# Kernel tuning notes

Hardware: AMD Instinct MI355X
Metric: run time of the kernel (lower is better)

The kernel has to match this reference:

```python
import jax, jax.numpy as jnp
import numpy as np

N_NODES = 100000
N_EDGES = 3200000
N_GRAPHS = 256
DIMS = [38, 64, 32, 16]


def setup_inputs() -> dict:
    key = jax.random.key(0)
    ks = jax.random.split(key, 16)
    x = jax.random.normal(ks[0], (N_NODES, DIMS[0]), dtype=jnp.float32)
    edge_index = jax.random.randint(ks[1], (2, N_EDGES), 0, N_NODES, dtype=jnp.int64)
    batch_vec = jnp.sort(jax.random.randint(ks[2], (N_NODES,), 0, N_GRAPHS, dtype=jnp.int64))
    inp = {"x": x, "edge_index": edge_index, "batch_vec": batch_vec}
    # Per layer l: W_rel [out,in] (with bias b [out]), W_root [out,in] (no bias)
    ki = 3
    for l in range(3):
        din, dout = DIMS[l], DIMS[l + 1]
        s = 1.0 / np.sqrt(din)
        inp[f"W_rel{l}"] = jax.random.uniform(ks[ki], (dout, din), minval=-s, maxval=s, dtype=jnp.float32); ki += 1
        inp[f"b{l}"] = jax.random.uniform(ks[ki], (dout,), minval=-s, maxval=s, dtype=jnp.float32); ki += 1
        inp[f"W_root{l}"] = jax.random.uniform(ks[ki], (dout, din), minval=-s, maxval=s, dtype=jnp.float32); ki += 1
    return inp


def _graph_conv(x, src, dst, W_rel, b, W_root):
    # sum_{j -> i} x_j, then linear (equivalent to summing transformed messages)
    agg = jax.ops.segment_sum(x[src], dst, num_segments=N_NODES)  # [N, din]
    return agg @ W_rel.T + b + x @ W_root.T


def reference(x, edge_index, batch_vec, W_rel0, b0, W_root0, W_rel1, b1, W_root1, W_rel2, b2, W_root2):
    src, dst = edge_index[0], edge_index[1]
    h = jnp.tanh(_graph_conv(x, src, dst, W_rel0, b0, W_root0))
    h = jnp.tanh(_graph_conv(h, src, dst, W_rel1, b1, W_root1))
    h = _graph_conv(h, src, dst, W_rel2, b2, W_root2)
    # global mean pool over graphs
    sums = jax.ops.segment_sum(h, batch_vec, num_segments=N_GRAPHS)  # [G, 16]
    counts = jax.ops.segment_sum(jnp.ones((N_NODES,), dtype=h.dtype), batch_vec, num_segments=N_GRAPHS)
    pooled = sums / jnp.maximum(counts, 1.0)[:, None]
    return jnp.tanh(pooled)
```

## Files before the change

### kernel.cpp

```cpp
#include <hip/hip_runtime.h>
#include <math.h>

#define N_NODES  100000
#define N_EDGES  3200000
#define N_GRAPHS 256


#define BSHIFT 9
#define NB 196
#define CAP 18432
#define NBLK 640
#define EPB ((N_EDGES + NBLK - 1) / NBLK)

typedef _Float16 f16;
typedef _Float16 f16x2 __attribute__((ext_vector_type(2)));

__device__ __forceinline__ float fast_tanh(float x) {
    x = fminf(20.f, fmaxf(-20.f, x));
    float e = __expf(2.f * x);
    return (e - 1.f) / (e + 1.f);
}

__device__ __forceinline__ unsigned int pack_bf2(float a, float b) {
    unsigned int ua = __float_as_uint(a);
    unsigned int ub = __float_as_uint(b);
    ua += 0x7fffu + ((ua >> 16) & 1u);
    ub += 0x7fffu + ((ub >> 16) & 1u);
    return (ua >> 16) | (ub & 0xffff0000u);
}

__device__ __forceinline__ f16x2 u2h(unsigned int u) { union { unsigned int u; f16x2 h; } c; c.u = u; return c.h; }
__device__ __forceinline__ unsigned int h2u(f16x2 h) { union { unsigned int u; f16x2 h; } c; c.h = h; return c.u; }
__device__ __forceinline__ unsigned int mkh2(float a, float b) {
    f16x2 v; v.x = (f16)a; v.y = (f16)b; return h2u(v);
}

__device__ __forceinline__ float fdot2f(f16x2 a, f16x2 b, float c) {
#if __has_builtin(__builtin_amdgcn_fdot2)
    return __builtin_amdgcn_fdot2(a, b, c, false);
#else
    return c + (float)a.x * (float)b.x + (float)a.y * (float)b.y;
#endif
}

__global__ __launch_bounds__(256) void k_scatter2(const int* __restrict__ src,
                                                  const int* __restrict__ dst,
                                                  int* __restrict__ bucket_cnt,
                                                  int* __restrict__ ebuf) {
    __shared__ int hist[NB];
    __shared__ int base[NB];
    __shared__ int cur[NB];
    int tid = threadIdx.x, b = blockIdx.x;
    for (int i = tid; i < NB; i += 256) { hist[i] = 0; cur[i] = 0; }
    __syncthreads();
    int lo = b * EPB, hi = min(lo + EPB, N_EDGES);
    for (int e = lo + tid; e < hi; e += 256)
        atomicAdd(&hist[((unsigned int)dst[e]) >> BSHIFT], 1);
    __syncthreads();
    for (int i = tid; i < NB; i += 256) {
        int c = hist[i];
        base[i] = (c > 0) ? atomicAdd(&bucket_cnt[i], c) : 0;
    }
    __syncthreads();
    for (int e = lo + tid; e < hi; e += 256) {
        int d = dst[e];
        int s = __builtin_nontemporal_load(src + e);
        int bin = d >> BSHIFT;
        int r = base[bin] + atomicAdd(&cur[bin], 1);
        if (r < CAP) ebuf[bin * CAP + r] = s | ((d & 511) << 17);
    }
}

__global__ __launch_bounds__(512) void k_bucket_csr2(const int* __restrict__ bucket_cnt,
                                                     int* __restrict__ ebuf,
                                                     int* __restrict__ rowptr,
                                                     int* __restrict__ rowend) {
    __shared__ int stage[CAP];
    __shared__ int cnt[512];
    __shared__ int cur[512];
    int b = blockIdx.x;
    int tid = threadIdx.x;
    int base = b * CAP;
    int n = min(bucket_cnt[b], CAP);
    cnt[tid] = 0;
    cur[tid] = 0;
    __syncthreads();
    for (int j = tid; j < n; j += 512) {
        int w = __builtin_nontemporal_load(ebuf + base + j);
        stage[j] = w;
        atomicAdd(&cnt[((unsigned int)w) >> 17], 1);
    }
    __syncthreads();
    int v = cnt[tid];
    int val = v;
    __syncthreads();
    cnt[tid] = val;
    __syncthreads();
#pragma unroll
    for (int o = 1; o < 512; o <<= 1) {
        int t = (tid >= o) ? cnt[tid - o] : 0;
        __syncthreads();
        val += t;
        cnt[tid] = val;
        __syncthreads();
    }
    int excl = val - v;
    int node = (b << BSHIFT) + tid;
    if (node < N_NODES) {
        rowptr[node] = base + excl;
        rowend[node] = base + val;
    }
    __syncthreads();
    for (int j = tid; j < n; j += 512) {
        int w = stage[j];
        int dl = ((unsigned int)w) >> 17;
        int off = (dl == 0) ? 0 : cnt[dl - 1];
        int r = atomicAdd(&cur[dl], 1);
        ebuf[base + off + r] = w & 0x1FFFF;
    }
}

__global__ __launch_bounds__(256) void k_cast_pad(const float* __restrict__ in,
                                                  unsigned int* __restrict__ out) {
    int i = blockIdx.x * 256 + threadIdx.x;
    if (i >= N_NODES * 20) return;
    int n = i / 20;
    int p = i - n * 20;
    unsigned int w = 0;
    if (p < 19) {
        float2 v = ((const float2*)in)[n * 19 + p];
        w = pack_bf2(v.x, v.y);
    }
    out[i] = w;
}

template<int NQ, int RSTRIDE, int ASTRIDE>
__global__ __launch_bounds__(256) void k_gather_quad(const unsigned int* __restrict__ feat,
                                                     const int* __restrict__ rowptr,
                                                     const int* __restrict__ rowend,
                                                     const int* __restrict__ elist,
                                                     float* __restrict__ agg) {
    int idx = blockIdx.x * 256 + threadIdx.x;
    if (idx >= N_NODES * NQ) return;
    int n = idx / NQ;
    int q = idx - n * NQ;
    int j = rowptr[n];
    int e = rowend[n];
    const unsigned int* fq = feat + q * 4;
    float a0 = 0.f, a1 = 0.f, a2 = 0.f, a3 = 0.f, a4 = 0.f, a5 = 0.f, a6 = 0.f, a7 = 0.f;
    for (; j + 3 < e; j += 4) {
        int s0 = __builtin_nontemporal_load(elist + j);
        int s1 = __builtin_nontemporal_load(elist + j + 1);
        int s2 = __builtin_nontemporal_load(elist + j + 2);
        int s3 = __builtin_nontemporal_load(elist + j + 3);
        uint4 w0 = *(const uint4*)(fq + (size_t)s0 * RSTRIDE);
        uint4 w1 = *(const uint4*)(fq + (size_t)s1 * RSTRIDE);
        uint4 w2 = *(const uint4*)(fq + (size_t)s2 * RSTRIDE);
        uint4 w3 = *(const uint4*)(fq + (size_t)s3 * RSTRIDE);
        a0 += __uint_as_float(w0.x << 16);
        a1 += __uint_as_float(w0.x & 0xffff0000u);
        a2 += __uint_as_float(w0.y << 16);
        a3 += __uint_as_float(w0.y & 0xffff0000u);
        a4 += __uint_as_float(w0.z << 16);
        a5 += __uint_as_float(w0.z & 0xffff0000u);
        a6 += __uint_as_float(w0.w << 16);
        a7 += __uint_as_float(w0.w & 0xffff0000u);
        a0 += __uint_as_float(w1.x << 16);
        a1 += __uint_as_float(w1.x & 0xffff0000u);
        a2 += __uint_as_float(w1.y << 16);
        a3 += __uint_as_float(w1.y & 0xffff0000u);
        a4 += __uint_as_float(w1.z << 16);
        a5 += __uint_as_float(w1.z & 0xffff0000u);
        a6 += __uint_as_float(w1.w << 16);
        a7 += __uint_as_float(w1.w & 0xffff0000u);
        a0 += __uint_as_float(w2.x << 16);
        a1 += __uint_as_float(w2.x & 0xffff0000u);
        a2 += __uint_as_float(w2.y << 16);
        a3 += __uint_as_float(w2.y & 0xffff0000u);
        a4 += __uint_as_float(w2.z << 16);
        a5 += __uint_as_float(w2.z & 0xffff0000u);
        a6 += __uint_as_float(w2.w << 16);
        a7 += __uint_as_float(w2.w & 0xffff0000u);
        a0 += __uint_as_float(w3.x << 16);
        a1 += __uint_as_float(w3.x & 0xffff0000u);
        a2 += __uint_as_float(w3.y << 16);
        a3 += __uint_as_float(w3.y & 0xffff0000u);
        a4 += __uint_as_float(w3.z << 16);
        a5 += __uint_as_float(w3.z & 0xffff0000u);
        a6 += __uint_as_float(w3.w << 16);
        a7 += __uint_as_float(w3.w & 0xffff0000u);
    }
    for (; j < e; ++j) {
        int s = __builtin_nontemporal_load(elist + j);
        uint4 w = *(const uint4*)(fq + (size_t)s * RSTRIDE);
        a0 += __uint_as_float(w.x << 16);
        a1 += __uint_as_float(w.x & 0xffff0000u);
        a2 += __uint_as_float(w.y << 16);
        a3 += __uint_as_float(w.y & 0xffff0000u);
        a4 += __uint_as_float(w.z << 16);
        a5 += __uint_as_float(w.z & 0xffff0000u);
        a6 += __uint_as_float(w.w << 16);
        a7 += __uint_as_float(w.w & 0xffff0000u);
    }
    float4* ao = (float4*)(agg + (size_t)n * ASTRIDE + q * 8);
    ao[0] = make_float4(a0, a1, a2, a3);
    ao[1] = make_float4(a4, a5, a6, a7);
}

__global__ __launch_bounds__(256) void k_fused0(const float* __restrict__ agg,
                                                const float* __restrict__ x,
                                                const float* __restrict__ Wrel0,
                                                const float* __restrict__ b0,
                                                const float* __restrict__ Wroot0,
                                                const float* __restrict__ Wrel1,
                                                const float* __restrict__ b1,
                                                const float* __restrict__ Wroot1,
                                                unsigned int* __restrict__ y1b,
                                                float* __restrict__ r1) {
    __shared__ unsigned int sWr[64 * 20];
    __shared__ unsigned int sWt[64 * 20];
    __shared__ unsigned int sW1r[32 * 32];
    __shared__ unsigned int sW1t[32 * 32];
    __shared__ float sb0[64];
    __shared__ float sb1[32];
    int tid = threadIdx.x;
    for (int i = tid; i < 64 * 20; i += 256) {
        int o = i / 20, d = i - o * 20;
        float a0 = (2 * d     < 38) ? Wrel0[o * 38 + 2 * d]     : 0.f;
        float a1 = (2 * d + 1 < 38) ? Wrel0[o * 38 + 2 * d + 1] : 0.f;
        float t0 = (2 * d     < 38) ? Wroot0[o * 38 + 2 * d]     : 0.f;
        float t1 = (2 * d + 1 < 38) ? Wroot0[o * 38 + 2 * d + 1] : 0.f;
        sWr[i] = mkh2(a0, a1);
        sWt[i] = mkh2(t0, t1);
    }
    for (int i = tid; i < 32 * 32; i += 256) {
        int op = i >> 5, j = i & 31;
        sW1r[i] = mkh2(Wrel1[j * 64 + 2 * op], Wrel1[j * 64 + 2 * op + 1]);
        sW1t[i] = mkh2(Wroot1[j * 64 + 2 * op], Wroot1[j * 64 + 2 * op + 1]);
    }
    if (tid < 64) sb0[tid] = b0[tid];
    if (tid < 32) sb1[tid] = b1[tid];
    __syncthreads();

    int lane = tid & 63;
    int ph = lane & 31;
    int sh = lane >> 5;
    int n0 = blockIdx.x * 256 + (tid >> 6) * 64 + 2 * ph;
    if (n0 >= N_NODES) return;
    int n1 = n0 + 1;

    unsigned int xa0[20], xx0[20], xa1[20], xx1[20];
    {
        const float2* A0 = (const float2*)(agg + (size_t)n0 * 40);
        const float2* X0 = (const float2*)(x   + (size_t)n0 * 38);
        const float2* A1 = (const float2*)(agg + (size_t)n1 * 40);
        const float2* X1 = (const float2*)(x   + (size_t)n1 * 38);
#pragma unroll
        for (int i = 0; i < 19; ++i) {
            float2 v;
            v = A0[i]; xa0[i] = mkh2(v.x, v.y);
            v = X0[i]; xx0[i] = mkh2(v.x, v.y);
            v = A1[i]; xa1[i] = mkh2(v.x, v.y);
            v = X1[i]; xx1[i] = mkh2(v.x, v.y);
        }
        xa0[19] = 0; xx0[19] = 0; xa1[19] = 0; xx1[19] = 0;
    }

    unsigned int hp0[16], hp1[16];
    int obase = sh * 32;
#pragma unroll
    for (int i = 0; i < 16; ++i) {
        float h00 = 0.f, h01 = 0.f, h10 = 0.f, h11 = 0.f;
#pragma unroll
        for (int par = 0; par < 2; ++par) {
            int o = obase + 2 * i + par;
            float c0 = sb0[o], c1 = 0.f, c2 = 0.f, c3 = 0.f;
            float d0 = sb0[o], d1 = 0.f, d2 = 0.f, d3 = 0.f;
            const uint4* wr = (const uint4*)(sWr + o * 20);
            const uint4* wt = (const uint4*)(sWt + o * 20);
#pragma unroll
            for (int q = 0; q < 5; ++q) {
                uint4 w = wr[q];
                c0 = fdot2f(u2h(xa0[4 * q + 0]), u2h(w.x), c0);
                c1 = fdot2f(u2h(xa0[4 * q + 1]), u2h(w.y), c1);
                c2 = fdot2f(u2h(xa0[4 * q + 2]), u2h(w.z), c2);
                c3 = fdot2f(u2h(xa0[4 * q + 3]), u2h(w.w), c3);
                d0 = fdot2f(u2h(xa1[4 * q + 0]), u2h(w.x), d0);
                d1 = fdot2f(u2h(xa1[4 * q + 1]), u2h(w.y), d1);
                d2 = fdot2f(u2h(xa1[4 * q + 2]), u2h(w.z), d2);
                d3 = fdot2f(u2h(xa1[4 * q + 3]), u2h(w.w), d3);
                uint4 v = wt[q];
                c0 = fdot2f(u2h(xx0[4 * q + 0]), u2h(v.x), c0);
                c1 = fdot2f(u2h(xx0[4 * q + 1]), u2h(v.y), c1);
                c2 = fdot2f(u2h(xx0[4 * q + 2]), u2h(v.z), c2);
                c3 = fdot2f(u2h(xx0[4 * q + 3]), u2h(v.w), c3);
                d0 = fdot2f(u2h(xx1[4 * q + 0]), u2h(v.x), d0);
                d1 = fdot2f(u2h(xx1[4 * q + 1]), u2h(v.y), d1);
                d2 = fdot2f(u2h(xx1[4 * q + 2]), u2h(v.z), d2);
                d3 = fdot2f(u2h(xx1[4 * q + 3]), u2h(v.w), d3);
            }
            float hA = fast_tanh(c0 + c1 + c2 + c3);
            float hB = fast_tanh(d0 + d1 + d2 + d3);
            if (par == 0) { h00 = hA; h10 = hB; }
            else          { h01 = hA; h11 = hB; }
        }
        hp0[i] = mkh2(h00, h01);
        hp1[i] = mkh2(h10, h11);
    }

    unsigned int H0[32], H1[32];
#pragma unroll
    for (int i = 0; i < 16; ++i) {
        unsigned int g0 = (unsigned int)__shfl_xor((int)hp0[i], 32);
        unsigned int g1 = (unsigned int)__shfl_xor((int)hp1[i], 32);
        if (sh == 0) { H0[i] = hp0[i]; H0[16 + i] = g0; H1[i] = hp1[i]; H1[16 + i] = g1; }
        else         { H0[i] = g0; H0[16 + i] = hp0[i]; H1[i] = g1; H1[16 + i] = hp1[i]; }
    }

    int jb = sh * 16;
    float y0[16], r0[16], y1v[16], r1v[16];
#pragma unroll
    for (int j = 0; j < 16; ++j) {
        y0[j] = 0.f; y1v[j] = 0.f;
        float bb = sb1[jb + j];
        r0[j] = bb; r1v[j] = bb;
    }
#pragma unroll
    for (int op = 0; op < 32; ++op) {
        f16x2 h0 = u2h(H0[op]);
        f16x2 h1 = u2h(H1[op]);
        const uint4* w1 = (const uint4*)(sW1r + op * 32 + jb);
        const uint4* w2 = (const uint4*)(sW1t + op * 32 + jb);
#pragma unroll
        for (int q = 0; q < 4; ++q) {
            uint4 a = w1[q], b = w2[q];
            y0[4 * q + 0] = fdot2f(h0, u2h(a.x), y0[4 * q + 0]);
            y0[4 * q + 1] = fdot2f(h0, u2h(a.y), y0[4 * q + 1]);
            y0[4 * q + 2] = fdot2f(h0, u2h(a.z), y0[4 * q + 2]);
            y0[4 * q + 3] = fdot2f(h0, u2h(a.w), y0[4 * q + 3]);
            y1v[4 * q + 0] = fdot2f(h1, u2h(a.x), y1v[4 * q + 0]);
            y1v[4 * q + 1] = fdot2f(h1, u2h(a.y), y1v[4 * q + 1]);
            y1v[4 * q + 2] = fdot2f(h1, u2h(a.z), y1v[4 * q + 2]);
            y1v[4 * q + 3] = fdot2f(h1, u2h(a.w), y1v[4 * q + 3]);
            r0[4 * q + 0] = fdot2f(h0, u2h(b.x), r0[4 * q + 0]);
            r0[4 * q + 1] = fdot2f(h0, u2h(b.y), r0[4 * q + 1]);
            r0[4 * q + 2] = fdot2f(h0, u2h(b.z), r0[4 * q + 2]);
            r0[4 * q + 3] = fdot2f(h0, u2h(b.w), r0[4 * q + 3]);
            r1v[4 * q + 0] = fdot2f(h1, u2h(b.x), r1v[4 * q + 0]);
            r1v[4 * q + 1] = fdot2f(h1, u2h(b.y), r1v[4 * q + 1]);
            r1v[4 * q + 2] = fdot2f(h1, u2h(b.z), r1v[4 * q + 2]);
            r1v[4 * q + 3] = fdot2f(h1, u2h(b.w), r1v[4 * q + 3]);
        }
    }

    unsigned int* yo0 = y1b + (size_t)n0 * 16 + 8 * sh;
    unsigned int* yo1 = y1b + (size_t)n1 * 16 + 8 * sh;
#pragma unroll
    for (int p = 0; p < 8; ++p) {
        yo0[p] = pack_bf2(y0[2 * p], y0[2 * p + 1]);
        yo1[p] = pack_bf2(y1v[2 * p], y1v[2 * p + 1]);
    }
    float4* ro0 = (float4*)(r1 + (size_t)n0 * 32 + jb);
    float4* ro1 = (float4*)(r1 + (size_t)n1 * 32 + jb);
#pragma unroll
    for (int q = 0; q < 4; ++q) {
        ro0[q] = make_float4(r0[4 * q], r0[4 * q + 1], r0[4 * q + 2], r0[4 * q + 3]);
        ro1[q] = make_float4(r1v[4 * q], r1v[4 * q + 1], r1v[4 * q + 2], r1v[4 * q + 3]);
    }
}

__global__ __launch_bounds__(256) void k_fused1(const float* __restrict__ agg,
                                                const float* __restrict__ r1,
                                                const float* __restrict__ Wrel2,
                                                float* __restrict__ h2,
                                                unsigned int* __restrict__ y2b)
{
    __shared__ float sW[32 * 16];
    int tid = threadIdx.x;
    for (int i = tid; i < 512; i += 256) {
        int k = i >> 4, j = i & 15;
        sW[i] = Wrel2[j * 32 + k];
    }
    __syncthreads();
    int n = blockIdx.x * 256 + tid;
    if (n >= N_NODES) return;
    const float4* a4 = (const float4*)(agg + (size_t)n * 32);
    const float4* r4 = (const float4*)(r1 + (size_t)n * 32);
    float h[32];
#pragma unroll
    for (int i = 0; i < 8; ++i) {
        float4 a = a4[i], r = r4[i];
        h[4 * i]     = fast_tanh(a.x + r.x);
        h[4 * i + 1] = fast_tanh(a.y + r.y);
        h[4 * i + 2] = fast_tanh(a.z + r.z);
        h[4 * i + 3] = fast_tanh(a.w + r.w);
    }
    float4* ho = (float4*)(h2 + (size_t)n * 32);
#pragma unroll
    for (int i = 0; i < 8; ++i) ho[i] = make_float4(h[4 * i], h[4 * i + 1], h[4 * i + 2], h[4 * i + 3]);
    float y[16];
#pragma unroll
    for (int j = 0; j < 16; ++j) y[j] = 0.f;
#pragma unroll
    for (int k = 0; k < 32; ++k) {
        const float4* w = (const float4*)(sW + k * 16);
#pragma unroll
        for (int j = 0; j < 4; ++j) {
            float4 wv = w[j];
            y[4 * j]     += h[k] * wv.x; y[4 * j + 1] += h[k] * wv.y;
            y[4 * j + 2] += h[k] * wv.z; y[4 * j + 3] += h[k] * wv.w;
        }
    }
    unsigned int* yo = y2b + (size_t)n * 8;
#pragma unroll
    for (int p = 0; p < 8; ++p) yo[p] = pack_bf2(y[2 * p], y[2 * p + 1]);
}

__global__ __launch_bounds__(256) void k_graph_start(const int* __restrict__ batch,
                                                     int* __restrict__ gstart) {
    int i = blockIdx.x * 256 + threadIdx.x;
    if (i >= N_NODES) return;
    int g = batch[i];
    int gp = (i == 0) ? -1 : batch[i - 1];
    for (int gg = gp + 1; gg <= g; ++gg) gstart[gg] = i;
    if (i == N_NODES - 1)
        for (int gg = g + 1; gg <= N_GRAPHS; ++gg) gstart[gg] = N_NODES;
}

__global__ __launch_bounds__(256) void k_pool(const float* __restrict__ agg,
                                              const float* __restrict__ h2,
                                              const int* __restrict__ gstart,
                                              float* __restrict__ psum)
{
    __shared__ float part[4][48];
    int g = blockIdx.x;
    int wave = threadIdx.x >> 6;
    int lane = threadIdx.x & 63;
    int s = gstart[g], e = gstart[g + 1];
    if (lane < 48) {
        float a0 = 0.f, a1 = 0.f;
        if (lane < 16) {
            int n = s + wave;
            for (; n + 4 < e; n += 8) {
                a0 += agg[n * 16 + lane];
                a1 += agg[(n + 4) * 16 + lane];
            }
            if (n < e) a0 += agg[n * 16 + lane];
        } else {
            int d = lane - 16;
            int n = s + wave;
            for (; n + 4 < e; n += 8) {
                a0 += h2[n * 32 + d];
                a1 += h2[(n + 4) * 32 + d];
            }
            if (n < e) a0 += h2[n * 32 + d];
        }
        part[wave][lane] = a0 + a1;
    }
    __syncthreads();
    if (threadIdx.x < 48)
        psum[g * 48 + threadIdx.x] = part[0][threadIdx.x] + part[1][threadIdx.x]
                                   + part[2][threadIdx.x] + part[3][threadIdx.x];
}

__global__ __launch_bounds__(256) void k_finalize2(const float* __restrict__ psum,
                                                   const float* __restrict__ Wroot,
                                                   const float* __restrict__ b,
                                                   const int* __restrict__ gstart,
                                                   float* __restrict__ out) {
    __shared__ float sW[16 * 32];
    __shared__ float sb[16];
    int tid = threadIdx.x;
    for (int i = tid; i < 16 * 32; i += 256) sW[i] = Wroot[i];
    if (tid < 16) sb[tid] = b[tid];
    __syncthreads();
    int idx = blockIdx.x * 256 + tid;
    if (idx >= N_GRAPHS * 16) return;
    int g = idx >> 4;
    int o = idx & 15;
    float cnt = (float)(gstart[g + 1] - gstart[g]);
    const float* p = psum + g * 48;
    float acc = p[o] + cnt * sb[o];
#pragma unroll
    for (int k = 0; k < 32; ++k) acc += p[16 + k] * sW[o * 32 + k];
    out[idx] = fast_tanh(acc / fmaxf(cnt, 1.f));
}

extern "C" void kernel_launch(void* const* d_in, const int* in_sizes, int n_in,
                              void* d_out, int out_size, void* d_ws, size_t ws_size,
                              hipStream_t stream) {
    const float* x      = (const float*)d_in[0];
    const int*   eidx   = (const int*)d_in[1];
    const int*   src    = eidx;
    const int*   dst    = eidx + N_EDGES;
    const int*   batch  = (const int*)d_in[2];
    const float* Wrel0  = (const float*)d_in[3];
    const float* b0     = (const float*)d_in[4];
    const float* Wroot0 = (const float*)d_in[5];
    const float* Wrel1  = (const float*)d_in[6];
    const float* b1     = (const float*)d_in[7];
    const float* Wroot1 = (const float*)d_in[8];
    const float* Wrel2  = (const float*)d_in[9];
    const float* b2     = (const float*)d_in[10];
    const float* Wroot2 = (const float*)d_in[11];
    float* out = (float*)d_out;

    float* ws   = (float*)d_ws;
    float* agg  = ws;
    float* r1   = agg + (size_t)N_NODES * 40;
    float* h2   = r1  + (size_t)N_NODES * 32;
    unsigned int* ybuf = (unsigned int*)(h2 + (size_t)N_NODES * 32);
    float* psum = (float*)(ybuf + (size_t)N_NODES * 16);
    int* rowptr      = (int*)(psum + N_GRAPHS * 48);
    int* rowend      = rowptr + N_NODES;
    int* gstart      = rowend + N_NODES;
    int* bucket_cnt  = gstart + 260;
    int* ebuf        = bucket_cnt + 400;
    unsigned int* xb = (unsigned int*)r1;
    unsigned int* y1b = ybuf;
    unsigned int* y2b = ybuf;

    k_cast_pad<<<(N_NODES * 20 + 255) / 256, 256, 0, stream>>>(x, xb);

    hipMemsetAsync(bucket_cnt, 0, sizeof(int) * NB, stream);
    k_scatter2<<<NBLK, 256, 0, stream>>>(src, dst, bucket_cnt, ebuf);
    k_bucket_csr2<<<NB, 512, 0, stream>>>(bucket_cnt, ebuf, rowptr, rowend);
    k_graph_start<<<(N_NODES + 255) / 256, 256, 0, stream>>>(batch, gstart);

    k_gather_quad<5, 20, 40><<<(N_NODES * 5 + 255) / 256, 256, 0, stream>>>(xb, rowptr, rowend, ebuf, agg);
    k_fused0<<<(N_NODES + 255) / 256, 256, 0, stream>>>(agg, x, Wrel0, b0, Wroot0,
                                                        Wrel1, b1, Wroot1, y1b, r1);

    k_gather_quad<4, 16, 32><<<(N_NODES * 4 + 255) / 256, 256, 0, stream>>>(y1b, rowptr, rowend, ebuf, agg);
    k_fused1<<<(N_NODES + 255) / 256, 256, 0, stream>>>(agg, r1, Wrel2, h2, y2b);

    k_gather_quad<2, 8, 16><<<(N_NODES * 2 + 255) / 256, 256, 0, stream>>>(y2b, rowptr, rowend, ebuf, agg);

    k_pool<<<N_GRAPHS, 256, 0, stream>>>(agg, h2, gstart, psum);
    k_finalize2<<<(N_GRAPHS * 16 + 255) / 256, 256, 0, stream>>>(psum, Wroot2, b2, gstart, out);
}
```

Baseline: 349.7 us.

## Split gathered feature tables into column slices for cache-resident gathers

Node feature tables for the first two layers are stored as separate column slices (32-byte rows), and each gather pass runs once per slice. Each pass therefore touches a smaller table (about 3.2 MB) that fits better in L2/MALL, so random gathers hit cache more often than with the 80/64-byte interleaved rows. The cost is extra kernel launches and repeated reads of the CSR edge list. Aggregate outputs now use nontemporal scalar stores instead of float4 stores.

```diff
diff --git a/kernel.cpp b/kernel.cpp
--- a/kernel.cpp
+++ b/kernel.cpp
@@ -120,8 +120,10 @@
     }
 }
 
-__global__ __launch_bounds__(256) void k_cast_pad(const float* __restrict__ in,
-                                                  unsigned int* __restrict__ out) {
+__global__ __launch_bounds__(256) void k_cast_slices(const float* __restrict__ in,
+                                                     unsigned int* __restrict__ sA,
+                                                     unsigned int* __restrict__ sB,
+                                                     unsigned int* __restrict__ sC) {
     int i = blockIdx.x * 256 + threadIdx.x;
     if (i >= N_NODES * 20) return;
     int n = i / 20;
@@ -131,10 +133,12 @@
         float2 v = ((const float2*)in)[n * 19 + p];
         w = pack_bf2(v.x, v.y);
     }
-    out[i] = w;
-}
-
-template<int NQ, int RSTRIDE, int ASTRIDE>
+    if (p < 8)       sA[n * 8 + p] = w;
+    else if (p < 16) sB[n * 8 + p - 8] = w;
+    else             sC[n * 4 + p - 16] = w;
+}
+
+template<int NQ, int RSTRIDE, int ASTRIDE, int OFF>
 __global__ __launch_bounds__(256) void k_gather_quad(const unsigned int* __restrict__ feat,
                                                      const int* __restrict__ rowptr,
                                                      const int* __restrict__ rowend,
@@ -202,9 +206,15 @@
         a6 += __uint_as_float(w.w << 16);
         a7 += __uint_as_float(w.w & 0xffff0000u);
     }
-    float4* ao = (float4*)(agg + (size_t)n * ASTRIDE + q * 8);
-    ao[0] = make_float4(a0, a1, a2, a3);
-    ao[1] = make_float4(a4, a5, a6, a7);
+    float* ao = agg + (size_t)n * ASTRIDE + OFF + q * 8;
+    __builtin_nontemporal_store(a0, ao + 0);
+    __builtin_nontemporal_store(a1, ao + 1);
+    __builtin_nontemporal_store(a2, ao + 2);
+    __builtin_nontemporal_store(a3, ao + 3);
+    __builtin_nontemporal_store(a4, ao + 4);
+    __builtin_nontemporal_store(a5, ao + 5);
+    __builtin_nontemporal_store(a6, ao + 6);
+    __builtin_nontemporal_store(a7, ao + 7);
 }
 
 __global__ __launch_bounds__(256) void k_fused0(const float* __restrict__ agg,
@@ -215,7 +225,8 @@
                                                 const float* __restrict__ Wrel1,
                                                 const float* __restrict__ b1,
                                                 const float* __restrict__ Wroot1,
-                                                unsigned int* __restrict__ y1b,
+                                                unsigned int* __restrict__ y1b0,
+                                                unsigned int* __restrict__ y1b1,
                                                 float* __restrict__ r1) {
     __shared__ unsigned int sWr[64 * 20];
     __shared__ unsigned int sWt[64 * 20];
@@ -353,8 +364,8 @@
         }
     }
 
-    unsigned int* yo0 = y1b + (size_t)n0 * 16 + 8 * sh;
-    unsigned int* yo1 = y1b + (size_t)n1 * 16 + 8 * sh;
+    unsigned int* yo0 = (sh ? y1b1 : y1b0) + (size_t)n0 * 8;
+    unsigned int* yo1 = (sh ? y1b1 : y1b0) + (size_t)n1 * 8;
 #pragma unroll
     for (int p = 0; p < 8; ++p) {
         yo0[p] = pack_bf2(y0[2 * p], y0[2 * p + 1]);
@@ -516,25 +527,31 @@
     int* gstart      = rowend + N_NODES;
     int* bucket_cnt  = gstart + 260;
     int* ebuf        = bucket_cnt + 400;
-    unsigned int* xb = (unsigned int*)r1;
-    unsigned int* y1b = ybuf;
-    unsigned int* y2b = ybuf;
-
-    k_cast_pad<<<(N_NODES * 20 + 255) / 256, 256, 0, stream>>>(x, xb);
+    unsigned int* xbA = (unsigned int*)r1;
+    unsigned int* xbB = xbA + (size_t)N_NODES * 8;
+    unsigned int* xbC = xbB + (size_t)N_NODES * 8;
+    unsigned int* y1b0 = ybuf;
+    unsigned int* y1b1 = ybuf + (size_t)N_NODES * 8;
+    unsigned int* y2b  = ybuf;
+
+    k_cast_slices<<<(N_NODES * 20 + 255) / 256, 256, 0, stream>>>(x, xbA, xbB, xbC);
 
     hipMemsetAsync(bucket_cnt, 0, sizeof(int) * NB, stream);
     k_scatter2<<<NBLK, 256, 0, stream>>>(src, dst, bucket_cnt, ebuf);
     k_bucket_csr2<<<NB, 512, 0, stream>>>(bucket_cnt, ebuf, rowptr, rowend);
     k_graph_start<<<(N_NODES + 255) / 256, 256, 0, stream>>>(batch, gstart);
 
-    k_gather_quad<5, 20, 40><<<(N_NODES * 5 + 255) / 256, 256, 0, stream>>>(xb, rowptr, rowend, ebuf, agg);
+    k_gather_quad<2, 8, 40, 0 ><<<(N_NODES * 2 + 255) / 256, 256, 0, stream>>>(xbA, rowptr, rowend, ebuf, agg);
+    k_gather_quad<2, 8, 40, 16><<<(N_NODES * 2 + 255) / 256, 256, 0, stream>>>(xbB, rowptr, rowend, ebuf, agg);
+    k_gather_quad<1, 4, 40, 32><<<(N_NODES * 1 + 255) / 256, 256, 0, stream>>>(xbC, rowptr, rowend, ebuf, agg);
     k_fused0<<<(N_NODES + 255) / 256, 256, 0, stream>>>(agg, x, Wrel0, b0, Wroot0,
-                                                        Wrel1, b1, Wroot1, y1b, r1);
-
-    k_gather_quad<4, 16, 32><<<(N_NODES * 4 + 255) / 256, 256, 0, stream>>>(y1b, rowptr, rowend, ebuf, agg);
+                                                        Wrel1, b1, Wroot1, y1b0, y1b1, r1);
+
+    k_gather_quad<2, 8, 32, 0 ><<<(N_NODES * 2 + 255) / 256, 256, 0, stream>>>(y1b0, rowptr, rowend, ebuf, agg);
+    k_gather_quad<2, 8, 32, 16><<<(N_NODES * 2 + 255) / 256, 256, 0, stream>>>(y1b1, rowptr, rowend, ebuf, agg);
     k_fused1<<<(N_NODES + 255) / 256, 256, 0, stream>>>(agg, r1, Wrel2, h2, y2b);
 
-    k_gather_quad<2, 8, 16><<<(N_NODES * 2 + 255) / 256, 256, 0, stream>>>(y2b, rowptr, rowend, ebuf, agg);
+    k_gather_quad<2, 8, 16, 0 ><<<(N_NODES * 2 + 255) / 256, 256, 0, stream>>>(y2b, rowptr, rowend, ebuf, agg);
 
     k_pool<<<N_GRAPHS, 256, 0, stream>>>(agg, h2, gstart, psum);
     k_finalize2<<<(N_GRAPHS * 16 + 255) / 256, 256, 0, stream>>>(psum, Wroot2, b2, gstart, out);
```

Result: slower. 452.7 us (+29.5%).
